# Kernel tuning notes

Hardware: AMD Instinct MI355X
Metric: run time of the kernel (lower is better)

The kernel has to match this reference:

```python
import jax, jax.numpy as jnp
import numpy as np
import math

B, S, D = 4, 1024, 1024
NH, HD = 16, 64
I = 4096
EPS = 1e-12


def layer_norm(x, g, b):
    mu = jnp.mean(x, axis=-1, keepdims=True)
    var = jnp.mean((x - mu) ** 2, axis=-1, keepdims=True)
    return (x - mu) * jax.lax.rsqrt(var + EPS) * g + b


def setup_inputs() -> dict:
    key = jax.random.key(0)
    ks = jax.random.split(key, 12)
    s = 0.02
    return {
        "hidden_states": jax.random.normal(ks[0], (B, S, D), jnp.float32),
        "attention_mask": jnp.zeros((B, 1, 1, S), jnp.float32),
        "Wq": jax.random.normal(ks[1], (D, D), jnp.float32) * s,
        "bq": jnp.zeros((D,), jnp.float32),
        "Wk": jax.random.normal(ks[2], (D, D), jnp.float32) * s,
        "bk": jnp.zeros((D,), jnp.float32),
        "Wv": jax.random.normal(ks[3], (D, D), jnp.float32) * s,
        "bv": jnp.zeros((D,), jnp.float32),
        "Wo": jax.random.normal(ks[4], (D, D), jnp.float32) * s,
        "bo": jnp.zeros((D,), jnp.float32),
        "ln1_g": jnp.ones((D,), jnp.float32),
        "ln1_b": jnp.zeros((D,), jnp.float32),
        "Wi": jax.random.normal(ks[5], (D, I), jnp.float32) * s,
        "bi": jnp.zeros((I,), jnp.float32),
        "Wout": jax.random.normal(ks[6], (I, D), jnp.float32) * s,
        "bout": jnp.zeros((D,), jnp.float32),
        "ln2_g": jnp.ones((D,), jnp.float32),
        "ln2_b": jnp.zeros((D,), jnp.float32),
    }


def reference(hidden_states, attention_mask, Wq, bq, Wk, bk, Wv, bv, Wo, bo,
              ln1_g, ln1_b, Wi, bi, Wout, bout, ln2_g, ln2_b):
    h = hidden_states
    # QKV projections, split into heads: [B,S,D] -> [B,NH,S,HD]
    def heads(x):
        return x.reshape(B, S, NH, HD).transpose(0, 2, 1, 3)
    q = heads(h @ Wq + bq)
    k = heads(h @ Wk + bk)
    v = heads(h @ Wv + bv)
    # manual attention: scores [B,NH,S,S]
    scores = jnp.einsum("bhqd,bhkd->bhqk", q, k) / math.sqrt(HD)
    scores = scores + attention_mask
    probs = jax.nn.softmax(scores, axis=-1)
    ctx = jnp.einsum("bhqk,bhkd->bhqd", probs, v)
    ctx = ctx.transpose(0, 2, 1, 3).reshape(B, S, D)
    # self-output: dense + residual + LN
    attn_out = layer_norm(ctx @ Wo + bo + h, ln1_g, ln1_b)
    # FFN: dense + exact gelu, dense + residual + LN
    inter = jax.nn.gelu(attn_out @ Wi + bi, approximate=False)
    out = layer_norm(inter @ Wout + bout + attn_out, ln2_g, ln2_b)
    return out
```

## Files before the change

### kernel.cpp

```cpp
#include <hip/hip_runtime.h>
#include <hip/hip_bf16.h>
#include <math.h>

#define B_ 4
#define S_ 1024
#define D_ 1024
#define NH_ 16
#define HD_ 64
#define I_ 4096
#define M_ (B_*S_)

typedef __bf16 bf16_8 __attribute__((ext_vector_type(8)));
typedef float f32x4 __attribute__((ext_vector_type(4)));
typedef unsigned short u16;

struct P4 { float* p[4]; };
struct T4 { const float* s[4]; u16* d[4]; };

__device__ __forceinline__ u16 f2b(float x) {
    __hip_bfloat16 h = __float2bfloat16(x);
    return *reinterpret_cast<u16*>(&h);
}

__device__ __forceinline__ void gload16(const void* g, void* l) {
    __builtin_amdgcn_global_load_lds(
        (const __attribute__((address_space(1))) void*)g,
        (__attribute__((address_space(3))) void*)l, 16, 0, 0);
}

__global__ __launch_bounds__(256) void cvt_bf16(
    const float4* __restrict__ in, ushort4* __restrict__ out, int n4)
{
    int i = blockIdx.x * 256 + threadIdx.x;
    if (i < n4) {
        float4 v = in[i];
        ushort4 o;
        o.x = f2b(v.x); o.y = f2b(v.y); o.z = f2b(v.z); o.w = f2b(v.w);
        out[i] = o;
    }
}

__global__ __launch_bounds__(256) void transpose_cvt(
    const float* __restrict__ in, u16* __restrict__ out, int K, int N)
{
    __shared__ float t[32][33];
    const int tid = threadIdx.x;
    const int k0 = blockIdx.y * 32, n0 = blockIdx.x * 32;
#pragma unroll
    for (int i = 0; i < 4; ++i) {
        int idx = i * 256 + tid;
        int r = idx >> 5, c = idx & 31;
        t[r][c] = in[(size_t)(k0 + r) * N + n0 + c];
    }
    __syncthreads();
    const int rr = tid >> 3, cc0 = (tid & 7) * 4;
    ushort4 o;
    o.x = f2b(t[cc0 + 0][rr]);
    o.y = f2b(t[cc0 + 1][rr]);
    o.z = f2b(t[cc0 + 2][rr]);
    o.w = f2b(t[cc0 + 3][rr]);
    *(ushort4*)(out + (size_t)(n0 + rr) * K + k0 + cc0) = o;
}

__global__ __launch_bounds__(256) void transpose4_cvt(T4 t4)
{
    __shared__ float t[32][33];
    const int tid = threadIdx.x;
    const int k0 = blockIdx.y * 32, n0 = blockIdx.x * 32;
    const float* in = t4.s[blockIdx.z];
    u16* out = t4.d[blockIdx.z];
#pragma unroll
    for (int i = 0; i < 4; ++i) {
        int idx = i * 256 + tid;
        int r = idx >> 5, c = idx & 31;
        t[r][c] = in[(size_t)(k0 + r) * D_ + n0 + c];
    }
    __syncthreads();
    const int rr = tid >> 3, cc0 = (tid & 7) * 4;
    ushort4 o;
    o.x = f2b(t[cc0 + 0][rr]);
    o.y = f2b(t[cc0 + 1][rr]);
    o.z = f2b(t[cc0 + 2][rr]);
    o.w = f2b(t[cc0 + 3][rr]);
    *(ushort4*)(out + (size_t)(n0 + rr) * D_ + k0 + cc0) = o;
}

#define NT_ 16

template<int MODE>
__global__ __launch_bounds__(512, 2) void gemm256(
    const u16* __restrict__ A, const u16* __restrict__ Bt,
    const float* __restrict__ b0, const float* __restrict__ b1,
    const float* __restrict__ b2,
    u16* __restrict__ outB, P4 parts, int N, int sA, int sB)
{
    __shared__ __align__(16) char sm[131072];

    const int tid  = threadIdx.x;
    const int lane = tid & 63, wid = tid >> 6;
    const int l15  = lane & 15, lg = lane >> 4;
    const int gm   = wid >> 2, gn = wid & 3;
    const int bm   = blockIdx.y * 256, bn = blockIdx.x * 256;
    const int koff = blockIdx.z * 1024;

    const int srow = (wid << 3) + (lane >> 3);
    const int skb  = ((lane & 7) << 4) ^ (((lane >> 3) & 7) << 4);
    const int scol = skb >> 1;
    const int xm   = (l15 & 7) << 4;

    f32x4 acc[8][4];
#pragma unroll
    for (int m = 0; m < 8; ++m)
#pragma unroll
        for (int j = 0; j < 4; ++j) {
            acc[m][j][0] = 0.f; acc[m][j][1] = 0.f;
            acc[m][j][2] = 0.f; acc[m][j][3] = 0.f;
        }

    auto stageA = [&](int v, int h) {
        const u16* src = A + (size_t)(bm + h * 128 + srow) * sA + koff + v * 64 + scol;
        char* dst = sm + ((v & 1) * 65536 + h * 16384 + wid * 1024);
        gload16(src, dst);
        gload16(src + (size_t)64 * sA, dst + 8192);
    };
    auto stageB = [&](int v, int h) {
        const u16* src = Bt + (size_t)(bn + h * 128 + srow) * sB + koff + v * 64 + scol;
        char* dst = sm + ((v & 1) * 65536 + 32768 + h * 16384 + wid * 1024);
        gload16(src, dst);
        gload16(src + (size_t)64 * sB, dst + 8192);
    };

    bf16_8 a[8], bb[2];
    auto loadA = [&](int vb, int s) {
        const char* base = sm + (vb * 65536 + gm * 16384);
#pragma unroll
        for (int m = 0; m < 8; ++m)
            a[m] = *(const bf16_8*)(base + (m * 16 + l15) * 128 +
                                    ((s * 64 + lg * 16) ^ xm));
    };
    auto loadB = [&](int vb, int s, int np) {
        const char* base = sm + (vb * 65536 + 32768 + (gn >> 1) * 16384);
#pragma unroll
        for (int j = 0; j < 2; ++j)
            bb[j] = *(const bf16_8*)(base + ((gn & 1) * 64 + (np * 2 + j) * 16 + l15) * 128 +
                                     ((s * 64 + lg * 16) ^ xm));
    };
    auto mfma16 = [&](int np) {
#pragma unroll
        for (int m = 0; m < 8; ++m)
#pragma unroll
            for (int j = 0; j < 2; ++j)
                acc[m][np * 2 + j] = __builtin_amdgcn_mfma_f32_16x16x32_bf16(
                    a[m], bb[j], acc[m][np * 2 + j], 0, 0, 0);
    };

    stageA(0, 0); stageA(0, 1);
    stageB(0, 0); stageB(0, 1);
    stageA(1, 0); stageA(1, 1);
    asm volatile("s_waitcnt vmcnt(4)" ::: "memory");
    __builtin_amdgcn_sched_barrier(0);
    __builtin_amdgcn_s_barrier();

    for (int v = 0; v < NT_ - 2; ++v) {
        const int vb = v & 1;
        loadA(vb, 0); loadB(vb, 0, 0);
        stageB(v + 1, 0); stageB(v + 1, 1);
        __builtin_amdgcn_s_barrier();
        asm volatile("s_waitcnt lgkmcnt(0)" ::: "memory");
        __builtin_amdgcn_s_setprio(1); mfma16(0); __builtin_amdgcn_s_setprio(0);
        __builtin_amdgcn_s_barrier();
        loadB(vb, 0, 1);
        __builtin_amdgcn_s_barrier();
        asm volatile("s_waitcnt lgkmcnt(0)" ::: "memory");
        __builtin_amdgcn_s_setprio(1); mfma16(1); __builtin_amdgcn_s_setprio(0);
        __builtin_amdgcn_s_barrier();
        loadA(vb, 1); loadB(vb, 1, 0);
        __builtin_amdgcn_s_barrier();
        asm volatile("s_waitcnt lgkmcnt(0)" ::: "memory");
        __builtin_amdgcn_s_setprio(1); mfma16(0); __builtin_amdgcn_s_setprio(0);
        __builtin_amdgcn_s_barrier();
        loadB(vb, 1, 1);
        stageA(v + 2, 0); stageA(v + 2, 1);
        __builtin_amdgcn_s_barrier();
        asm volatile("s_waitcnt lgkmcnt(0)" ::: "memory");
        __builtin_amdgcn_s_setprio(1); mfma16(1); __builtin_amdgcn_s_setprio(0);
        asm volatile("s_waitcnt vmcnt(4)" ::: "memory");
        __builtin_amdgcn_sched_barrier(0);
        __builtin_amdgcn_s_barrier();
    }
    {
        const int vb = (NT_ - 2) & 1;
        loadA(vb, 0); loadB(vb, 0, 0);
        stageB(NT_ - 1, 0); stageB(NT_ - 1, 1);
        __builtin_amdgcn_s_barrier();
        asm volatile("s_waitcnt lgkmcnt(0)" ::: "memory");
        __builtin_amdgcn_s_setprio(1); mfma16(0); __builtin_amdgcn_s_setprio(0);
        __builtin_amdgcn_s_barrier();
        loadB(vb, 0, 1);
        __builtin_amdgcn_s_barrier();
        asm volatile("s_waitcnt lgkmcnt(0)" ::: "memory");
        __builtin_amdgcn_s_setprio(1); mfma16(1); __builtin_amdgcn_s_setprio(0);
        __builtin_amdgcn_s_barrier();
        loadA(vb, 1); loadB(vb, 1, 0);
        __builtin_amdgcn_s_barrier();
        asm volatile("s_waitcnt lgkmcnt(0)" ::: "memory");
        __builtin_amdgcn_s_setprio(1); mfma16(0); __builtin_amdgcn_s_setprio(0);
        __builtin_amdgcn_s_barrier();
        loadB(vb, 1, 1);
        __builtin_amdgcn_s_barrier();
        asm volatile("s_waitcnt lgkmcnt(0)" ::: "memory");
        __builtin_amdgcn_s_setprio(1); mfma16(1); __builtin_amdgcn_s_setprio(0);
        asm volatile("s_waitcnt vmcnt(0)" ::: "memory");
        __builtin_amdgcn_sched_barrier(0);
        __builtin_amdgcn_s_barrier();
    }
    {
        const int vb = (NT_ - 1) & 1;
        loadA(vb, 0); loadB(vb, 0, 0); mfma16(0);
        loadB(vb, 0, 1);               mfma16(1);
        loadA(vb, 1); loadB(vb, 1, 0); mfma16(0);
        loadB(vb, 1, 1);               mfma16(1);
    }

    if (MODE == 2) {
        float* oP = parts.p[blockIdx.z];
#pragma unroll
        for (int m = 0; m < 8; ++m)
#pragma unroll
            for (int r = 0; r < 4; ++r) {
                const int row = bm + gm * 128 + m * 16 + lg * 4 + r;
#pragma unroll
                for (int j = 0; j < 4; ++j)
                    oP[(size_t)row * N + bn + gn * 64 + j * 16 + l15] = acc[m][j][r];
            }
    } else {
        const int cg = (bn + gn * 64) >> 10;
        const float* bp = (MODE == 0) ? (cg == 0 ? b0 : cg == 1 ? b1 : b2) : b0;
        const int cbase = (MODE == 0) ? ((bn + gn * 64) & 1023) : (bn + gn * 64);
        float bs[4];
#pragma unroll
        for (int j = 0; j < 4; ++j) bs[j] = bp[cbase + j * 16 + l15];
#pragma unroll
        for (int m = 0; m < 8; ++m)
#pragma unroll
            for (int r = 0; r < 4; ++r) {
                const int row = bm + gm * 128 + m * 16 + lg * 4 + r;
#pragma unroll
                for (int j = 0; j < 4; ++j) {
                    float v = acc[m][j][r] + bs[j];
                    if (MODE == 1)
                        v = 0.5f * v * (1.0f + erff(v * 0.70710678118654752f));
                    outB[(size_t)row * N + bn + gn * 64 + j * 16 + l15] = f2b(v);
                }
            }
    }
}

__global__ __launch_bounds__(256) void gemm_splitk(
    const u16* __restrict__ A, const u16* __restrict__ Bt,
    P4 parts, int N, int K, int kchunk)
{
    __shared__ __align__(16) u16 As[128 * 32];
    __shared__ __align__(16) u16 Bs[128 * 32];

    const int tid  = threadIdx.x;
    const int lane = tid & 63, wid = tid >> 6;
    const int l15  = lane & 15, lg = lane >> 4;
    const int wm   = (wid >> 1) * 64, wn = (wid & 1) * 64;
    const int bm   = blockIdx.y * 128, bn = blockIdx.x * 128;
    const int wbase16 = (tid & ~63) * 16;
    const int kt0 = blockIdx.z * kchunk, kt1 = kt0 + kchunk;
    float* outP = parts.p[blockIdx.z];

    const int r0 = tid >> 2;
    const int c0 = (tid & 3) * 8;

    f32x4 acc[4][4];
#pragma unroll
    for (int i = 0; i < 4; ++i)
#pragma unroll
        for (int j = 0; j < 4; ++j) {
            acc[i][j][0] = 0.f; acc[i][j][1] = 0.f;
            acc[i][j][2] = 0.f; acc[i][j][3] = 0.f;
        }

    for (int kt = kt0; kt < kt1; kt += 32) {
        __syncthreads();
        gload16(A  + (size_t)(bm + r0)      * K + kt + c0, (char*)As + wbase16);
        gload16(A  + (size_t)(bm + r0 + 64) * K + kt + c0, (char*)As + wbase16 + 4096);
        gload16(Bt + (size_t)(bn + r0)      * K + kt + c0, (char*)Bs + wbase16);
        gload16(Bt + (size_t)(bn + r0 + 64) * K + kt + c0, (char*)Bs + wbase16 + 4096);
        __syncthreads();

        bf16_8 af[4], bfr[4];
#pragma unroll
        for (int f = 0; f < 4; ++f) {
            af[f]  = *(const bf16_8*)((const char*)As + (wm + f * 16 + l15) * 64 + lg * 16);
            bfr[f] = *(const bf16_8*)((const char*)Bs + (wn + f * 16 + l15) * 64 + lg * 16);
        }
#pragma unroll
        for (int i = 0; i < 4; ++i)
#pragma unroll
            for (int j = 0; j < 4; ++j)
                acc[i][j] = __builtin_amdgcn_mfma_f32_16x16x32_bf16(
                    af[i], bfr[j], acc[i][j], 0, 0, 0);
    }

#pragma unroll
    for (int i = 0; i < 4; ++i)
#pragma unroll
        for (int r = 0; r < 4; ++r) {
            const int row = bm + wm + i * 16 + lg * 4 + r;
#pragma unroll
            for (int j = 0; j < 4; ++j)
                outP[(size_t)row * N + bn + wn + j * 16 + l15] = acc[i][j][r];
        }
}

template<int NPART>
__global__ __launch_bounds__(256) void ln_reduce(
    P4 parts, const float* __restrict__ bias, const float* __restrict__ res,
    const float* __restrict__ g, const float* __restrict__ b,
    float* __restrict__ O, u16* __restrict__ OB)
{
    const int row = blockIdx.x;
    const int tid = threadIdx.x;
    const size_t off = (size_t)row * D_ + tid * 4;

    float4 v = *(const float4*)(res + off);
    const float4 bi = *(const float4*)(bias + tid * 4);
    v.x += bi.x; v.y += bi.y; v.z += bi.z; v.w += bi.w;
#pragma unroll
    for (int p = 0; p < NPART; ++p) {
        const float4 t = *(const float4*)(parts.p[p] + off);
        v.x += t.x; v.y += t.y; v.z += t.z; v.w += t.w;
    }

    float s  = v.x + v.y + v.z + v.w;
    float sq = v.x * v.x + v.y * v.y + v.z * v.z + v.w * v.w;
#pragma unroll
    for (int o = 32; o; o >>= 1) {
        s  += __shfl_down(s, o);
        sq += __shfl_down(sq, o);
    }
    __shared__ float red[8];
    const int wid = tid >> 6, lane = tid & 63;
    if (lane == 0) { red[wid] = s; red[4 + wid] = sq; }
    __syncthreads();
    const float ts = red[0] + red[1] + red[2] + red[3];
    const float tq = red[4] + red[5] + red[6] + red[7];
    const float mu  = ts * (1.0f / D_);
    const float var = tq * (1.0f / D_) - mu * mu;
    const float rs  = rsqrtf(var + 1e-12f);

    const float4 gv = *(const float4*)(g + tid * 4);
    const float4 bv = *(const float4*)(b + tid * 4);
    float4 o;
    o.x = (v.x - mu) * rs * gv.x + bv.x;
    o.y = (v.y - mu) * rs * gv.y + bv.y;
    o.z = (v.z - mu) * rs * gv.z + bv.z;
    o.w = (v.w - mu) * rs * gv.w + bv.w;
    *(float4*)(O + off) = o;
    if (OB) {
        ushort4 ob;
        ob.x = f2b(o.x); ob.y = f2b(o.y); ob.z = f2b(o.z); ob.w = f2b(o.w);
        *(ushort4*)(OB + off) = ob;
    }
}

__global__ __launch_bounds__(256) void attn_mfma(
    const u16* __restrict__ Qb, const u16* __restrict__ Kb,
    const u16* __restrict__ Vb, const float* __restrict__ mask,
    u16* __restrict__ ctxb, int qs)
{
    __shared__ __align__(16) char sm[24576];
    char* Ksm = sm;
    char* Vsm = sm + 8192;

    const int tid  = threadIdx.x;
    const int lane = tid & 63, wid = tid >> 6;
    char* Psm = sm + 16384 + wid * 2048;
    const int l15 = lane & 15, lg = lane >> 4;
    const int h = blockIdx.y, b = blockIdx.z;
    const int q0 = blockIdx.x * 64 + wid * 16;
    const size_t inhead  = ((size_t)b * S_) * qs + (size_t)h * 64;
    const size_t outhead = ((size_t)b * S_) * D_ + (size_t)h * 64;

    const u16* Qrow = Qb + inhead + (size_t)(q0 + l15) * qs;
    const bf16_8 qf0 = *(const bf16_8*)(Qrow + lg * 8);
    const bf16_8 qf1 = *(const bf16_8*)(Qrow + 32 + lg * 8);

    f32x4 ctx[4];
#pragma unroll
    for (int i = 0; i < 4; ++i) { ctx[i][0]=0.f; ctx[i][1]=0.f; ctx[i][2]=0.f; ctx[i][3]=0.f; }
    float m_r = -1e30f, l_r = 0.f;

    const int skey = tid >> 2;
    const int sd0  = (tid & 3) * 16;
    const int xo_p = (l15 & 7) << 4;

    for (int kt = 0; kt < S_; kt += 64) {
        __syncthreads();
        {
            const u16* ks = Kb + inhead + (size_t)(kt + skey) * qs + sd0;
            const bf16_8 k0 = *(const bf16_8*)(ks);
            const bf16_8 k1 = *(const bf16_8*)(ks + 8);
            const int xo = (skey & 7) << 4;
            *(bf16_8*)(Ksm + skey * 128 + ((sd0 * 2)      ^ xo)) = k0;
            *(bf16_8*)(Ksm + skey * 128 + ((sd0 * 2 + 16) ^ xo)) = k1;

            const u16* vs = Vb + inhead + (size_t)(kt + skey) * qs + sd0;
            const bf16_8 v0 = *(const bf16_8*)(vs);
            const bf16_8 v1 = *(const bf16_8*)(vs + 8);
#pragma unroll
            for (int j = 0; j < 8; ++j) {
                const int d = sd0 + j;
                *(__bf16*)(Vsm + d * 128 + ((skey * 2) ^ ((d & 7) << 4))) = v0[j];
            }
#pragma unroll
            for (int j = 0; j < 8; ++j) {
                const int d = sd0 + 8 + j;
                *(__bf16*)(Vsm + d * 128 + ((skey * 2) ^ ((d & 7) << 4))) = v1[j];
            }
        }
        __syncthreads();

        f32x4 sc[4];
#pragma unroll
        for (int kf = 0; kf < 4; ++kf) {
            const int key = kf * 16 + l15;
            const int xo = (key & 7) << 4;
            f32x4 a; a[0]=0.f; a[1]=0.f; a[2]=0.f; a[3]=0.f;
            const bf16_8 kA = *(const bf16_8*)(Ksm + key * 128 + ((lg * 16)      ^ xo));
            a = __builtin_amdgcn_mfma_f32_16x16x32_bf16(kA, qf0, a, 0, 0, 0);
            const bf16_8 kB = *(const bf16_8*)(Ksm + key * 128 + ((64 + lg * 16) ^ xo));
            a = __builtin_amdgcn_mfma_f32_16x16x32_bf16(kB, qf1, a, 0, 0, 0);
            sc[kf] = a;
        }

        float p[16];
        float tmax = -1e30f;
#pragma unroll
        for (int kf = 0; kf < 4; ++kf) {
            const float4 mk = *(const float4*)(mask + (size_t)b * S_ + kt + kf * 16 + lg * 4);
#pragma unroll
            for (int r = 0; r < 4; ++r) {
                const float mkr = (r == 0) ? mk.x : (r == 1) ? mk.y : (r == 2) ? mk.z : mk.w;
                p[kf * 4 + r] = sc[kf][r] * 0.125f + mkr;
                tmax = fmaxf(tmax, p[kf * 4 + r]);
            }
        }
        tmax = fmaxf(tmax, __shfl_xor(tmax, 16));
        tmax = fmaxf(tmax, __shfl_xor(tmax, 32));

        const float mnew = fmaxf(m_r, tmax);
        const float scl  = __expf(m_r - mnew);
        m_r = mnew;

        float psum = 0.f;
#pragma unroll
        for (int i = 0; i < 16; ++i) {
            p[i] = __expf(p[i] - mnew);
            psum += p[i];
        }
        psum += __shfl_xor(psum, 16);
        psum += __shfl_xor(psum, 32);
        l_r = l_r * scl + psum;

#pragma unroll
        for (int fd = 0; fd < 4; ++fd)
#pragma unroll
            for (int r = 0; r < 4; ++r) ctx[fd][r] *= scl;

#pragma unroll
        for (int kf = 0; kf < 4; ++kf)
#pragma unroll
            for (int rr = 0; rr < 2; ++rr) {
                ushort2 wv;
                wv.x = f2b(p[kf * 4 + 2 * rr]);
                wv.y = f2b(p[kf * 4 + 2 * rr + 1]);
                *(ushort2*)(Psm + l15 * 128 +
                            (((kf * 16 + lg * 4 + 2 * rr) * 2) ^ xo_p)) = wv;
            }

        asm volatile("s_waitcnt lgkmcnt(0)" ::: "memory");

#pragma unroll
        for (int s = 0; s < 2; ++s) {
            const bf16_8 pf = *(const bf16_8*)(Psm + l15 * 128 +
                                ((s * 64 + lg * 16) ^ xo_p));
#pragma unroll
            for (int fd = 0; fd < 4; ++fd) {
                const int d = fd * 16 + l15;
                const bf16_8 vf = *(const bf16_8*)(Vsm + d * 128 +
                                    ((s * 64 + lg * 16) ^ ((d & 7) << 4)));
                ctx[fd] = __builtin_amdgcn_mfma_f32_16x16x32_bf16(vf, pf, ctx[fd], 0, 0, 0);
            }
        }
    }

    const float inv = 1.f / l_r;
    const size_t qrow = outhead + (size_t)(q0 + l15) * D_;
#pragma unroll
    for (int fd = 0; fd < 4; ++fd) {
        ushort4 o;
        o.x = f2b(ctx[fd][0] * inv);
        o.y = f2b(ctx[fd][1] * inv);
        o.z = f2b(ctx[fd][2] * inv);
        o.w = f2b(ctx[fd][3] * inv);
        *(ushort4*)(ctxb + qrow + fd * 16 + lg * 4) = o;
    }
}

extern "C" void kernel_launch(void* const* d_in, const int* in_sizes, int n_in,
                              void* d_out, int out_size, void* d_ws, size_t ws_size,
                              hipStream_t stream)
{
    const float* h    = (const float*)d_in[0];
    const float* mask = (const float*)d_in[1];
    const float* Wq   = (const float*)d_in[2];
    const float* bq   = (const float*)d_in[3];
    const float* Wk   = (const float*)d_in[4];
    const float* bk   = (const float*)d_in[5];
    const float* Wv   = (const float*)d_in[6];
    const float* bv   = (const float*)d_in[7];
    const float* Wo   = (const float*)d_in[8];
    const float* bo   = (const float*)d_in[9];
    const float* ln1g = (const float*)d_in[10];
    const float* ln1b = (const float*)d_in[11];
    const float* Wi   = (const float*)d_in[12];
    const float* bi   = (const float*)d_in[13];
    const float* Wout = (const float*)d_in[14];
    const float* bout = (const float*)d_in[15];
    const float* ln2g = (const float*)d_in[16];
    const float* ln2b = (const float*)d_in[17];
    float* out = (float*)d_out;

    char* w = (char*)d_ws;
    const size_t MiB = 1ull << 20;
    u16*   Woutt  = (u16*)(w + 0);
    float* attnF  = (float*)(w + 8 * MiB);
    float* woP0   = attnF;
    float* woP1   = (float*)(w + 24 * MiB);
    u16*   interB = (u16*)(w + 24 * MiB);
    u16*   hb     = (u16*)(w + 56 * MiB);
    float* ffP0   = (float*)(w + 56 * MiB);
    u16*   Wqkvt  = (u16*)(w + 64 * MiB);
    u16*   Wot    = (u16*)(w + 70 * MiB);
    float* ffP1   = (float*)(w + 72 * MiB);
    u16*   Wit    = (u16*)(w + 72 * MiB);
    float* ffP2   = (float*)(w + 88 * MiB);
    u16*   QKVb   = (u16*)(w + 80 * MiB);
    u16*   ctxb   = (u16*)(w + 104 * MiB);
    float* ffP3   = (float*)(w + 104 * MiB);
    u16*   attnB  = (u16*)(w + 112 * MiB);

    const dim3 blk(256);
    P4 zp; zp.p[0] = zp.p[1] = zp.p[2] = zp.p[3] = nullptr;

    cvt_bf16<<<dim3((M_ * D_ / 4) / 256), blk, 0, stream>>>(
        (const float4*)h, (ushort4*)hb, M_ * D_ / 4);
    T4 t4;
    t4.s[0] = Wq; t4.s[1] = Wk; t4.s[2] = Wv; t4.s[3] = Wo;
    t4.d[0] = Wqkvt; t4.d[1] = Wqkvt + 1024 * 1024;
    t4.d[2] = Wqkvt + 2 * 1024 * 1024; t4.d[3] = Wot;
    transpose4_cvt<<<dim3(32, 32, 4), blk, 0, stream>>>(t4);
    transpose_cvt<<<dim3(128, 32), blk, 0, stream>>>(Wi,   Wit,   D_, I_);
    transpose_cvt<<<dim3(32, 128), blk, 0, stream>>>(Wout, Woutt, I_, D_);

    gemm256<0><<<dim3(12, 16, 1), dim3(512), 0, stream>>>(
        hb, Wqkvt, bq, bk, bv, QKVb, zp, 3072, 1024, 1024);

    attn_mfma<<<dim3(S_ / 64, NH_, B_), blk, 0, stream>>>(
        QKVb, QKVb + 1024, QKVb + 2048, mask, ctxb, 3072);

    P4 woP; woP.p[0] = woP0; woP.p[1] = woP1; woP.p[2] = nullptr; woP.p[3] = nullptr;
    gemm_splitk<<<dim3(8, 32, 2), blk, 0, stream>>>(ctxb, Wot, woP, D_, D_, 512);
    ln_reduce<2><<<dim3(M_), blk, 0, stream>>>(woP, bo, h, ln1g, ln1b, attnF, attnB);

    gemm256<1><<<dim3(16, 16, 1), dim3(512), 0, stream>>>(
        attnB, Wit, bi, nullptr, nullptr, interB, zp, 4096, 1024, 1024);

    P4 ffP; ffP.p[0] = ffP0; ffP.p[1] = ffP1; ffP.p[2] = ffP2; ffP.p[3] = ffP3;
    gemm256<2><<<dim3(4, 16, 4), dim3(512), 0, stream>>>(
        interB, Woutt, nullptr, nullptr, nullptr, nullptr, ffP, 1024, 4096, 4096);
    ln_reduce<4><<<dim3(M_), blk, 0, stream>>>(ffP, bout, attnF, ln2g, ln2b, out, nullptr);
}
```

Measured before the change: 239.0 us.

## Restructure attention staging with transposed LDS reads, prefetch, and tanh-form GELU

The attention kernel now uses 512-thread blocks covering 128 queries. Block indices are swizzled to map workgroups onto (batch, head, query block). K/V tiles are prefetched into registers one iteration ahead, and V is stored untransposed and read with ds_read_b64_tr_b16, replacing scalar transposed LDS stores. Separately, the exact erf GELU in the FFN up-projection epilogue is replaced by a sigmoid/tanh approximation using fast exp and divide, which changes numerics relative to the exact-gelu reference.

```diff
diff --git a/kernel.cpp b/kernel.cpp
--- a/kernel.cpp
+++ b/kernel.cpp
@@ -12,6 +12,7 @@
 
 typedef __bf16 bf16_8 __attribute__((ext_vector_type(8)));
 typedef float f32x4 __attribute__((ext_vector_type(4)));
+typedef unsigned int u32x2 __attribute__((ext_vector_type(2)));
 typedef unsigned short u16;
 
 struct P4 { float* p[4]; };
@@ -248,8 +249,10 @@
 #pragma unroll
                 for (int j = 0; j < 4; ++j) {
                     float v = acc[m][j][r] + bs[j];
-                    if (MODE == 1)
-                        v = 0.5f * v * (1.0f + erff(v * 0.70710678118654752f));
+                    if (MODE == 1) {
+                        const float u = v * (1.5957691216f + 0.0713548163f * v * v);
+                        v = __fdividef(v, 1.0f + __expf(-u));
+                    }
                     outB[(size_t)row * N + bn + gn * 64 + j * 16 + l15] = f2b(v);
                 }
             }
@@ -368,12 +371,12 @@
     }
 }
 
-__global__ __launch_bounds__(256) void attn_mfma(
+__global__ __launch_bounds__(512) void attn_mfma(
     const u16* __restrict__ Qb, const u16* __restrict__ Kb,
     const u16* __restrict__ Vb, const float* __restrict__ mask,
     u16* __restrict__ ctxb, int qs)
 {
-    __shared__ __align__(16) char sm[24576];
+    __shared__ __align__(16) char sm[32768];
     char* Ksm = sm;
     char* Vsm = sm + 8192;
 
@@ -381,8 +384,14 @@
     const int lane = tid & 63, wid = tid >> 6;
     char* Psm = sm + 16384 + wid * 2048;
     const int l15 = lane & 15, lg = lane >> 4;
-    const int h = blockIdx.y, b = blockIdx.z;
-    const int q0 = blockIdx.x * 64 + wid * 16;
+
+    const int wg  = blockIdx.x;
+    const int swz = (wg & 7) * 64 + (wg >> 3);
+    const int b   = swz >> 7;
+    const int h   = (swz >> 3) & 15;
+    const int qb  = swz & 7;
+
+    const int q0 = qb * 128 + wid * 16;
     const size_t inhead  = ((size_t)b * S_) * qs + (size_t)h * 64;
     const size_t outhead = ((size_t)b * S_) * D_ + (size_t)h * 64;
 
@@ -395,45 +404,37 @@
     for (int i = 0; i < 4; ++i) { ctx[i][0]=0.f; ctx[i][1]=0.f; ctx[i][2]=0.f; ctx[i][3]=0.f; }
     float m_r = -1e30f, l_r = 0.f;
 
-    const int skey = tid >> 2;
-    const int sd0  = (tid & 3) * 16;
+    const int skey = tid >> 3;
+    const int sd0  = (tid & 7) * 8;
     const int xo_p = (l15 & 7) << 4;
-
-    for (int kt = 0; kt < S_; kt += 64) {
+    const int kwoff = skey * 128 + ((sd0 * 2) ^ ((skey & 7) << 4));
+    const int vwoff = (sd0 >> 4) * 2048 + skey * 32 + ((sd0 & 8) << 1);
+
+    const __attribute__((address_space(3))) char* vtr =
+        (const __attribute__((address_space(3))) char*)(Vsm + lg * 256 + l15 * 2);
+
+    bf16_8 kreg = *(const bf16_8*)(Kb + inhead + (size_t)skey * qs + sd0);
+    bf16_8 vreg = *(const bf16_8*)(Vb + inhead + (size_t)skey * qs + sd0);
+
+    for (int t = 0; t < S_ / 64; ++t) {
         __syncthreads();
-        {
-            const u16* ks = Kb + inhead + (size_t)(kt + skey) * qs + sd0;
-            const bf16_8 k0 = *(const bf16_8*)(ks);
-            const bf16_8 k1 = *(const bf16_8*)(ks + 8);
-            const int xo = (skey & 7) << 4;
-            *(bf16_8*)(Ksm + skey * 128 + ((sd0 * 2)      ^ xo)) = k0;
-            *(bf16_8*)(Ksm + skey * 128 + ((sd0 * 2 + 16) ^ xo)) = k1;
-
-            const u16* vs = Vb + inhead + (size_t)(kt + skey) * qs + sd0;
-            const bf16_8 v0 = *(const bf16_8*)(vs);
-            const bf16_8 v1 = *(const bf16_8*)(vs + 8);
-#pragma unroll
-            for (int j = 0; j < 8; ++j) {
-                const int d = sd0 + j;
-                *(__bf16*)(Vsm + d * 128 + ((skey * 2) ^ ((d & 7) << 4))) = v0[j];
-            }
-#pragma unroll
-            for (int j = 0; j < 8; ++j) {
-                const int d = sd0 + 8 + j;
-                *(__bf16*)(Vsm + d * 128 + ((skey * 2) ^ ((d & 7) << 4))) = v1[j];
-            }
-        }
+        *(bf16_8*)(Ksm + kwoff) = kreg;
+        *(bf16_8*)(Vsm + vwoff) = vreg;
         __syncthreads();
+        if (t < S_ / 64 - 1) {
+            const size_t noff = inhead + (size_t)((t + 1) * 64 + skey) * qs + sd0;
+            kreg = *(const bf16_8*)(Kb + noff);
+            vreg = *(const bf16_8*)(Vb + noff);
+        }
 
         f32x4 sc[4];
 #pragma unroll
         for (int kf = 0; kf < 4; ++kf) {
             const int key = kf * 16 + l15;
-            const int xo = (key & 7) << 4;
             f32x4 a; a[0]=0.f; a[1]=0.f; a[2]=0.f; a[3]=0.f;
-            const bf16_8 kA = *(const bf16_8*)(Ksm + key * 128 + ((lg * 16)      ^ xo));
+            const bf16_8 kA = *(const bf16_8*)(Ksm + key * 128 + ((lg * 16)      ^ xo_p));
             a = __builtin_amdgcn_mfma_f32_16x16x32_bf16(kA, qf0, a, 0, 0, 0);
-            const bf16_8 kB = *(const bf16_8*)(Ksm + key * 128 + ((64 + lg * 16) ^ xo));
+            const bf16_8 kB = *(const bf16_8*)(Ksm + key * 128 + ((64 + lg * 16) ^ xo_p));
             a = __builtin_amdgcn_mfma_f32_16x16x32_bf16(kB, qf1, a, 0, 0, 0);
             sc[kf] = a;
         }
@@ -442,7 +443,7 @@
         float tmax = -1e30f;
 #pragma unroll
         for (int kf = 0; kf < 4; ++kf) {
-            const float4 mk = *(const float4*)(mask + (size_t)b * S_ + kt + kf * 16 + lg * 4);
+            const float4 mk = *(const float4*)(mask + (size_t)b * S_ + t * 64 + kf * 16 + lg * 4);
 #pragma unroll
             for (int r = 0; r < 4; ++r) {
                 const float mkr = (r == 0) ? mk.x : (r == 1) ? mk.y : (r == 2) ? mk.z : mk.w;
@@ -482,20 +483,36 @@
                 *(ushort2*)(Psm + l15 * 128 +
                             (((kf * 16 + lg * 4 + 2 * rr) * 2) ^ xo_p)) = wv;
             }
-
         asm volatile("s_waitcnt lgkmcnt(0)" ::: "memory");
 
 #pragma unroll
         for (int s = 0; s < 2; ++s) {
             const bf16_8 pf = *(const bf16_8*)(Psm + l15 * 128 +
                                 ((s * 64 + lg * 16) ^ xo_p));
-#pragma unroll
-            for (int fd = 0; fd < 4; ++fd) {
-                const int d = fd * 16 + l15;
-                const bf16_8 vf = *(const bf16_8*)(Vsm + d * 128 +
-                                    ((s * 64 + lg * 16) ^ ((d & 7) << 4)));
-                ctx[fd] = __builtin_amdgcn_mfma_f32_16x16x32_bf16(vf, pf, ctx[fd], 0, 0, 0);
-            }
+            const __attribute__((address_space(3))) char* a3 = vtr + s * 1024;
+            u32x2 r0, r1, r2, r3, r4, r5, r6, r7;
+            asm volatile(
+                "ds_read_b64_tr_b16 %0, %8 offset:0\n\t"
+                "ds_read_b64_tr_b16 %1, %8 offset:128\n\t"
+                "ds_read_b64_tr_b16 %2, %8 offset:2048\n\t"
+                "ds_read_b64_tr_b16 %3, %8 offset:2176\n\t"
+                "ds_read_b64_tr_b16 %4, %8 offset:4096\n\t"
+                "ds_read_b64_tr_b16 %5, %8 offset:4224\n\t"
+                "ds_read_b64_tr_b16 %6, %8 offset:6144\n\t"
+                "ds_read_b64_tr_b16 %7, %8 offset:6272\n\t"
+                "s_waitcnt lgkmcnt(0)"
+                : "=&v"(r0), "=&v"(r1), "=&v"(r2), "=&v"(r3),
+                  "=&v"(r4), "=&v"(r5), "=&v"(r6), "=&v"(r7)
+                : "v"(a3));
+            union Cv { unsigned u[4]; bf16_8 v; };
+            Cv c0; c0.u[0] = r0.x; c0.u[1] = r0.y; c0.u[2] = r1.x; c0.u[3] = r1.y;
+            Cv c1; c1.u[0] = r2.x; c1.u[1] = r2.y; c1.u[2] = r3.x; c1.u[3] = r3.y;
+            Cv c2; c2.u[0] = r4.x; c2.u[1] = r4.y; c2.u[2] = r5.x; c2.u[3] = r5.y;
+            Cv c3; c3.u[0] = r6.x; c3.u[1] = r6.y; c3.u[2] = r7.x; c3.u[3] = r7.y;
+            ctx[0] = __builtin_amdgcn_mfma_f32_16x16x32_bf16(c0.v, pf, ctx[0], 0, 0, 0);
+            ctx[1] = __builtin_amdgcn_mfma_f32_16x16x32_bf16(c1.v, pf, ctx[1], 0, 0, 0);
+            ctx[2] = __builtin_amdgcn_mfma_f32_16x16x32_bf16(c2.v, pf, ctx[2], 0, 0, 0);
+            ctx[3] = __builtin_amdgcn_mfma_f32_16x16x32_bf16(c3.v, pf, ctx[3], 0, 0, 0);
         }
     }
 
@@ -571,7 +588,7 @@
     gemm256<0><<<dim3(12, 16, 1), dim3(512), 0, stream>>>(
         hb, Wqkvt, bq, bk, bv, QKVb, zp, 3072, 1024, 1024);
 
-    attn_mfma<<<dim3(S_ / 64, NH_, B_), blk, 0, stream>>>(
+    attn_mfma<<<dim3(512), dim3(512), 0, stream>>>(
         QKVb, QKVb + 1024, QKVb + 2048, mask, ctxb, 3072);
 
     P4 woP; woP.p[0] = woP0; woP.p[1] = woP1; woP.p[2] = nullptr; woP.p[3] = nullptr;
```

Measured after the change: 219.3 us. 8.2% less time.
